# Optimization experiments

Hardware: AMD Instinct MI355X
Metric: run time of the kernel (lower is better)

Reference implementation:

```python
import jax, jax.numpy as jnp
import numpy as np

H, W = 32, 64          # img_size
NB = 4                 # fno_blocks
SCALE = 0.02


def setup_inputs() -> dict:
    key = jax.random.key(0)
    ks = jax.random.split(key, 8)
    B, N, C = 16, H * W, 768
    BS = C // NB
    x = jax.random.normal(ks[0], (B, N, C), dtype=jnp.float32)
    w1 = SCALE * jax.random.normal(ks[1], (2, NB, BS, BS), dtype=jnp.float32)
    b1 = SCALE * jax.random.normal(ks[2], (2, NB, BS), dtype=jnp.float32)
    w2 = SCALE * jax.random.normal(ks[3], (2, NB, BS, BS), dtype=jnp.float32)
    b2 = SCALE * jax.random.normal(ks[4], (2, NB, BS), dtype=jnp.float32)
    # Conv1d(C, C, kernel_size=1) == per-token linear layer over channels
    bias_w = jax.random.normal(ks[5], (C, C), dtype=jnp.float32) / np.sqrt(C)
    bias_b = jax.random.normal(ks[6], (C,), dtype=jnp.float32) * 0.01
    return {"x": x, "w1": w1, "b1": b1, "w2": w2, "b2": b2,
            "bias_w": bias_w, "bias_b": bias_b}


def _mul(a, w):
    # block-diagonal matmul: a [..., NB, BS], w [NB, BS, BS]
    return jnp.einsum('...bd,bdk->...bk', a, w)


def reference(x, w1, b1, w2, b2, bias_w, bias_b):
    B, N, C = x.shape
    BS = C // NB
    # Conv1d kernel-size-1 bias path
    bias = x @ bias_w.T + bias_b
    # spatial FFT
    xf = jnp.fft.rfftn(x.reshape(B, H, W, C), axes=(1, 2), norm='ortho')
    xf = xf.reshape(B, H, W // 2 + 1, NB, BS)
    xr, xi = xf.real, xf.imag
    # layer 1 (complex block-diag matmul + bias, ReLU on real/imag separately)
    r1 = jax.nn.relu(_mul(xr, w1[0]) - _mul(xi, w1[1]) + b1[0])
    i1 = jax.nn.relu(_mul(xr, w1[1]) + _mul(xi, w1[0]) + b1[1])
    # layer 2 -- NOTE: imag part uses the *updated* real part, matching the
    # original torch code's in-place reassignment order.
    r2 = _mul(r1, w2[0]) - _mul(i1, w2[1]) + b2[0]
    i2 = _mul(r2, w2[1]) + _mul(i1, w2[0]) + b2[1]
    xc = jax.lax.complex(r2, i2).reshape(B, H, W // 2 + 1, C)
    out = jnp.fft.irfftn(xc, s=(H, W), axes=(1, 2), norm='ortho')
    return out.reshape(B, N, C) + bias
```

## Files before the change

kernel.cpp:

```cpp
#include <hip/hip_runtime.h>
#include <hip/hip_bf16.h>
#include <stdint.h>

#define BB 16
#define HH 32
#define WW 64
#define CC 768
#define W2C 33
#define ROWW (2*CC)

typedef __bf16 bf16x8 __attribute__((ext_vector_type(8)));
typedef float f32x4 __attribute__((ext_vector_type(4)));

__device__ __forceinline__ unsigned short f2bf(float f) {
  __hip_bfloat16 h = __float2bfloat16(f);
  return __builtin_bit_cast(unsigned short, h);
}
__device__ __forceinline__ float bf2f(unsigned short u) {
  union { unsigned int i; float f; } x;
  x.i = ((unsigned int)u) << 16;
  return x.f;
}

__device__ __forceinline__ void g2l16(const void* g, void* l) {
  __builtin_amdgcn_global_load_lds((const __attribute__((address_space(1))) unsigned int*)g,
                                   (__attribute__((address_space(3))) unsigned int*)l,
                                   16, 0, 0);
}

__device__ __host__ constexpr int brevc(int x, int bits) {
  int r = 0;
  for (int i = 0; i < bits; ++i) r |= ((x >> i) & 1) << (bits - 1 - i);
  return r;
}

constexpr double TPI = 6.283185307179586476925286766559;
constexpr double tsin_(double x) {
  double t = x, s = x, x2 = x * x;
  for (int i = 1; i < 14; ++i) { t *= -x2 / (double)((2 * i) * (2 * i + 1)); s += t; }
  return s;
}
constexpr double tcos_(double x) {
  double t = 1.0, s = 1.0, x2 = x * x;
  for (int i = 1; i < 14; ++i) { t *= -x2 / (double)((2 * i - 1) * (2 * i)); s += t; }
  return s;
}
struct Tw64 { float c[64]; float s[64]; };
constexpr Tw64 mk_tw() {
  Tw64 r{};
  for (int k = 0; k < 64; ++k) {
    int q = k >> 4, m = k & 15;
    double a = (TPI / 64.0) * m;
    double cq = tcos_(a), sq = tsin_(a);
    double c, s;
    if (q == 0)      { c =  cq; s =  sq; }
    else if (q == 1) { c = -sq; s =  cq; }
    else if (q == 2) { c = -cq; s = -sq; }
    else             { c =  sq; s = -cq; }
    r.c[k] = (float)c;
    r.s[k] = (float)(-s);
  }
  return r;
}
constexpr Tw64 TW = mk_tw();

template<int N, bool INV>
__device__ __forceinline__ void fft_reg(float2 (&v)[N]) {
  constexpr int LOG2N = (N == 64) ? 6 : 5;
#pragma unroll
  for (int s = 0; s < LOG2N; ++s) {
    const int len = N >> s;
    const int half = len >> 1;
    const int tstep = 64 / len;
#pragma unroll
    for (int i = 0; i < N; i += len) {
#pragma unroll
      for (int j = 0; j < half; ++j) {
        float2 u = v[i + j];
        float2 t = v[i + j + half];
        float sr = u.x + t.x, si = u.y + t.y;
        float dr = u.x - t.x, di = u.y - t.y;
        float wr = TW.c[j * tstep];
        float wi = INV ? -TW.s[j * tstep] : TW.s[j * tstep];
        v[i + j] = make_float2(sr, si);
        v[i + j + half] = make_float2(dr * wr - di * wi, dr * wi + di * wr);
      }
    }
  }
}

__global__ __launch_bounds__(128) void fft_fwd_w(const float* __restrict__ x,
                                                 ushort2* __restrict__ yw,
                                                 unsigned short* __restrict__ xb) {
  __shared__ __align__(16) float xs[32][128];
  const int t = threadIdx.x;
  const int bh = blockIdx.x;
  const int c0 = blockIdx.y * 128;
  const float* xrow = x + (size_t)bh * (WW * CC) + c0;
  unsigned short* xbrow = xb + (size_t)bh * (WW * CC) + c0;
  const int rg = t >> 5;
  const int lc = (t & 31) * 4;
  float2 v[32];
#pragma unroll
  for (int half = 0; half < 2; ++half) {
    if (half) __syncthreads();
    float4 f[8];
#pragma unroll
    for (int it = 0; it < 8; ++it)
      f[it] = *(const float4*)(xrow + (size_t)(half * 32 + it * 4 + rg) * CC + lc);
#pragma unroll
    for (int it = 0; it < 8; ++it) {
      *(float4*)&xs[it * 4 + rg][lc] = f[it];
      *(ushort4*)(xbrow + (size_t)(half * 32 + it * 4 + rg) * CC + lc) =
          make_ushort4(f2bf(f[it].x), f2bf(f[it].y), f2bf(f[it].z), f2bf(f[it].w));
    }
    __syncthreads();
#pragma unroll
    for (int n = 0; n < 16; ++n)
      v[half * 16 + n] = make_float2(xs[2 * n][t], xs[2 * n + 1][t]);
  }
  fft_reg<32, false>(v);
  ushort2* yp = yw + (size_t)bh * (W2C * CC) + c0 + t;
  {
    float2 Z0 = v[0];
    yp[0] = make_ushort2(f2bf(Z0.x + Z0.y), f2bf(0.f));
    yp[(size_t)32 * CC] = make_ushort2(f2bf(Z0.x - Z0.y), f2bf(0.f));
  }
#pragma unroll
  for (int k = 1; k < 32; ++k) {
    float2 Zk = v[brevc(k, 5)];
    float2 Zm = v[brevc(32 - k, 5)];
    float Er = 0.5f * (Zk.x + Zm.x), Ei = 0.5f * (Zk.y - Zm.y);
    float Odr = 0.5f * (Zk.y + Zm.y), Odi = -0.5f * (Zk.x - Zm.x);
    float wx = TW.c[k], wy = TW.s[k];
    float Xr = Er + wx * Odr - wy * Odi;
    float Xi = Ei + wx * Odi + wy * Odr;
    yp[(size_t)k * CC] = make_ushort2(f2bf(Xr), f2bf(Xi));
  }
}

__global__ __launch_bounds__(256) void fft_fwd_h(const ushort2* __restrict__ yw,
                                                 unsigned short* __restrict__ xf) {
  const int bk = blockIdx.x;
  const int b = bk / W2C, kw = bk - b * W2C;
  const int c = blockIdx.y * 256 + threadIdx.x;
  const ushort2* yp = yw + ((size_t)b * HH * W2C + kw) * CC + c;
  float2 v[32];
#pragma unroll
  for (int h = 0; h < 32; ++h) {
    ushort2 u = yp[(size_t)h * (W2C * CC)];
    v[h] = make_float2(bf2f(u.x), bf2f(u.y));
  }
  fft_reg<32, false>(v);
  const int nb = c / 192, cc = c - nb * 192;
  unsigned short* xp = xf + (size_t)nb * 384 + cc;
  const float s = 0.022097086912079608f;
#pragma unroll
  for (int kh = 0; kh < 32; ++kh) {
    float2 z = v[brevc(kh, 5)];
    size_t m = ((size_t)b * HH + kh) * W2C + kw;
    xp[m * ROWW] = f2bf(z.x * s);
    xp[m * ROWW + 192] = f2bf(z.y * s);
  }
}

__global__ __launch_bounds__(256) void fft_inv_h(const unsigned short* __restrict__ r2,
                                                 ushort2* __restrict__ g) {
  const int bk = blockIdx.x;
  const int b = bk / W2C, kw = bk - b * W2C;
  const int c = blockIdx.y * 256 + threadIdx.x;
  const int nb = c / 192, cc = c - nb * 192;
  const unsigned short* rp = r2 + (size_t)nb * 384 + cc;
  float2 v[32];
#pragma unroll
  for (int kh = 0; kh < 32; ++kh) {
    size_t m = ((size_t)b * HH + kh) * W2C + kw;
    v[kh] = make_float2(bf2f(rp[m * ROWW]), bf2f(rp[m * ROWW + 192]));
  }
  fft_reg<32, true>(v);
  ushort2* gp = g + ((size_t)b * HH * W2C + kw) * CC + c;
#pragma unroll
  for (int h = 0; h < 32; ++h) {
    float2 z = v[brevc(h, 5)];
    gp[(size_t)h * (W2C * CC)] = make_ushort2(f2bf(z.x), f2bf(z.y));
  }
}

__global__ __launch_bounds__(128) void fft_inv_w(const ushort2* __restrict__ g,
                                                 const unsigned short* __restrict__ biasb,
                                                 float* __restrict__ out) {
  __shared__ __align__(16) float ys[32][128];
  const int t = threadIdx.x;
  const int bh = blockIdx.x;
  const int c0 = blockIdx.y * 128;
  const ushort2* gp = g + (size_t)bh * (W2C * CC) + c0 + t;
  float2 v[32];
  {
    float X0 = bf2f(gp[0].x);
    float X32 = bf2f(gp[(size_t)32 * CC].x);
    v[0] = make_float2(0.5f * (X0 + X32), 0.5f * (X0 - X32));
  }
#pragma unroll
  for (int k = 1; k < 32; ++k) {
    ushort2 uk = gp[(size_t)k * CC];
    ushort2 um = gp[(size_t)(32 - k) * CC];
    float2 Xk = make_float2(bf2f(uk.x), bf2f(uk.y));
    float2 Xm = make_float2(bf2f(um.x), bf2f(um.y));
    float Ar = 0.5f * (Xk.x + Xm.x), Ai = 0.5f * (Xk.y - Xm.y);
    float Dr = 0.5f * (Xk.x - Xm.x), Di = 0.5f * (Xk.y + Xm.y);
    float wx = TW.c[k], wy = TW.s[k];
    float Br = wx * Dr + wy * Di;
    float Bi = wx * Di - wy * Dr;
    v[k] = make_float2(Ar - Bi, Ai + Br);
  }
  fft_reg<32, true>(v);
  const float s2 = 0.04419417382415922f;
  float* orow = out + (size_t)bh * (WW * CC) + c0;
  const unsigned short* brow = biasb + (size_t)bh * (WW * CC) + c0;
  const int rg = t >> 5;
  const int lc = (t & 31) * 4;
#pragma unroll
  for (int half = 0; half < 2; ++half) {
    if (half) __syncthreads();
    ushort4 b4[8];
#pragma unroll
    for (int it = 0; it < 8; ++it)
      b4[it] = *(const ushort4*)(brow + (size_t)(half * 32 + it * 4 + rg) * CC + lc);
#pragma unroll
    for (int n = 0; n < 16; ++n) {
      float2 z = v[brevc(half * 16 + n, 5)];
      ys[2 * n][t] = z.x * s2;
      ys[2 * n + 1][t] = z.y * s2;
    }
    __syncthreads();
#pragma unroll
    for (int it = 0; it < 8; ++it) {
      const int w = half * 32 + it * 4 + rg;
      float4 f = *(const float4*)&ys[it * 4 + rg][lc];
      f.x += bf2f(b4[it].x); f.y += bf2f(b4[it].y);
      f.z += bf2f(b4[it].z); f.w += bf2f(b4[it].w);
      *(float4*)(orow + (size_t)w * CC + lc) = f;
    }
  }
}

template<bool RELU, bool OBF>
__global__ __launch_bounds__(256) void gemm_bt(
    const unsigned short* __restrict__ A, int lda, int aZ,
    const unsigned short* __restrict__ Bw, int K, int bZ,
    const float* __restrict__ bias, int biasZ,
    void* __restrict__ outp, int ldo, int oZ) {
  __shared__ __align__(16) unsigned short As[128 * 32];
  __shared__ __align__(16) unsigned short Bs[128 * 32];
  const int t = threadIdx.x;
  const int z = blockIdx.z;
  const size_t m0 = (size_t)blockIdx.x * 128;
  const int n0 = blockIdx.y * 128;
  const unsigned short* Ap = A + m0 * lda + (size_t)z * aZ;
  const unsigned short* Bp = Bw + (size_t)n0 * K + (size_t)z * bZ;
  const int lane = t & 63, wave = t >> 6;
  const int lr = lane & 15, quad = lane >> 4;
  const int wm = (wave >> 1) * 64, wn = (wave & 1) * 64;
  const int row = t >> 2;
  const int sl = t & 3;
  const int kb = (sl ^ ((row >> 1) & 3)) * 8;
  const int swzf = (lr >> 1) & 3;
  f32x4 acc[4][4] = {};
  for (int k0 = 0; k0 < K; k0 += 32) {
    const unsigned short* ga = Ap + (size_t)row * lda + (k0 + kb);
    g2l16(ga, &As[row * 32 + sl * 8]);
    g2l16(ga + (size_t)64 * lda, &As[(row + 64) * 32 + sl * 8]);
    const unsigned short* gb = Bp + (size_t)row * K + (k0 + kb);
    g2l16(gb, &Bs[row * 32 + sl * 8]);
    g2l16(gb + (size_t)64 * K, &Bs[(row + 64) * 32 + sl * 8]);
    __syncthreads();
    bf16x8 af[4], bfr[4];
#pragma unroll
    for (int mi = 0; mi < 4; ++mi)
      af[mi] = *(const bf16x8*)&As[(wm + mi * 16 + lr) * 32 + ((quad ^ swzf) * 8)];
#pragma unroll
    for (int ni = 0; ni < 4; ++ni)
      bfr[ni] = *(const bf16x8*)&Bs[(wn + ni * 16 + lr) * 32 + ((quad ^ swzf) * 8)];
#pragma unroll
    for (int mi = 0; mi < 4; ++mi)
#pragma unroll
      for (int ni = 0; ni < 4; ++ni)
        acc[mi][ni] = __builtin_amdgcn_mfma_f32_16x16x32_bf16(af[mi], bfr[ni], acc[mi][ni], 0, 0, 0);
    __syncthreads();
  }
#pragma unroll
  for (int mi = 0; mi < 4; ++mi) {
    const size_t mrow = m0 + wm + mi * 16 + quad * 4;
#pragma unroll
    for (int ni = 0; ni < 4; ++ni) {
      const int ncol = n0 + wn + ni * 16 + lr;
      const float bv = bias[z * biasZ + ncol];
#pragma unroll
      for (int r = 0; r < 4; ++r) {
        float vv = acc[mi][ni][r] + bv;
        if (RELU) vv = fmaxf(vv, 0.f);
        const size_t off = (mrow + r) * (size_t)ldo + (size_t)z * oZ + ncol;
        if (OBF) ((unsigned short*)outp)[off] = f2bf(vv);
        else ((float*)outp)[off] = vv;
      }
    }
  }
}

__global__ __launch_bounds__(256) void cvt_bf16(const float* __restrict__ in,
                                                unsigned short* __restrict__ outp) {
  const size_t i = ((size_t)blockIdx.x * 256 + threadIdx.x) * 4;
  float4 v = *(const float4*)(in + i);
  ushort4 o = make_ushort4(f2bf(v.x), f2bf(v.y), f2bf(v.z), f2bf(v.w));
  *(ushort4*)(outp + i) = o;
}

__global__ __launch_bounds__(256) void build_w1(const float* __restrict__ w1,
                                                const float* __restrict__ b1,
                                                unsigned short* __restrict__ w1t,
                                                float* __restrict__ bias1) {
  const int idx = blockIdx.x * 256 + threadIdx.x;
  const int nb = idx / (384 * 384);
  const int rem = idx - nb * (384 * 384);
  const int n = rem / 384, k = rem - (rem / 384) * 384;
  const bool khi = k >= 192, nhi = n >= 192;
  const int kk = khi ? k - 192 : k, nn = nhi ? n - 192 : n;
  float val;
  if (!khi && !nhi)      val =  w1[((0 * 4 + nb) * 192 + kk) * 192 + nn];
  else if (khi && !nhi)  val = -w1[((1 * 4 + nb) * 192 + kk) * 192 + nn];
  else if (!khi && nhi)  val =  w1[((1 * 4 + nb) * 192 + kk) * 192 + nn];
  else                   val =  w1[((0 * 4 + nb) * 192 + kk) * 192 + nn];
  w1t[((size_t)nb * 384 + n) * 384 + k] = f2bf(val);
  if (k == 0)
    bias1[nb * 384 + n] = nhi ? b1[(1 * 4 + nb) * 192 + nn] : b1[(0 * 4 + nb) * 192 + nn];
}

__global__ __launch_bounds__(256) void build_w2(const float* __restrict__ w2,
                                                const float* __restrict__ b2,
                                                unsigned short* __restrict__ w2t,
                                                float* __restrict__ bias2) {
  const int idx = blockIdx.x * 256 + threadIdx.x;
  const int nb = idx / (384 * 384);
  const int rem = idx - nb * (384 * 384);
  const int n = rem / 384, k = rem - (rem / 384) * 384;
  const bool khi = k >= 192, nhi = n >= 192;
  const int kk = khi ? k - 192 : k, nn = nhi ? n - 192 : n;
  float val;
  if (!khi && !nhi) {
    val = w2[((0 * 4 + nb) * 192 + kk) * 192 + nn];
  } else if (khi && !nhi) {
    val = -w2[((1 * 4 + nb) * 192 + kk) * 192 + nn];
  } else if (!khi && nhi) {
    float s = 0.f;
    for (int d = 0; d < 192; ++d)
      s += w2[((0 * 4 + nb) * 192 + kk) * 192 + d] * w2[((1 * 4 + nb) * 192 + d) * 192 + nn];
    val = s;
  } else {
    float s = 0.f;
    for (int d = 0; d < 192; ++d)
      s += w2[((1 * 4 + nb) * 192 + kk) * 192 + d] * w2[((1 * 4 + nb) * 192 + d) * 192 + nn];
    val = w2[((0 * 4 + nb) * 192 + kk) * 192 + nn] - s;
  }
  w2t[((size_t)nb * 384 + n) * 384 + k] = f2bf(val);
  if (k == 0) {
    float bv;
    if (!nhi) {
      bv = b2[(0 * 4 + nb) * 192 + nn];
    } else {
      float s = 0.f;
      for (int d = 0; d < 192; ++d)
        s += b2[(0 * 4 + nb) * 192 + d] * w2[((1 * 4 + nb) * 192 + d) * 192 + nn];
      bv = b2[(1 * 4 + nb) * 192 + nn] + s;
    }
    bias2[nb * 384 + n] = bv;
  }
}

extern "C" void kernel_launch(void* const* d_in, const int* in_sizes, int n_in,
                              void* d_out, int out_size, void* d_ws, size_t ws_size,
                              hipStream_t stream) {
  (void)in_sizes; (void)n_in; (void)out_size; (void)ws_size;
  const float* x  = (const float*)d_in[0];
  const float* w1 = (const float*)d_in[1];
  const float* b1 = (const float*)d_in[2];
  const float* w2 = (const float*)d_in[3];
  const float* b2 = (const float*)d_in[4];
  const float* bw = (const float*)d_in[5];
  const float* bb = (const float*)d_in[6];
  float* out = (float*)d_out;

  char* p = (char*)d_ws;
  unsigned short* buf1 = (unsigned short*)p; p += 51904512;
  unsigned short* buf2 = (unsigned short*)p; p += 51904512;
  unsigned short* buf3 = (unsigned short*)p; p += 51904512;
  unsigned short* bwb  = (unsigned short*)p; p += 1179648;
  unsigned short* w1t  = (unsigned short*)p; p += 1179648;
  unsigned short* w2t  = (unsigned short*)p; p += 1179648;
  float* bias1 = (float*)p; p += 6144;
  float* bias2 = (float*)p; p += 6144;

  cvt_bf16<<<589824 / 1024, 256, 0, stream>>>(bw, bwb);
  build_w1<<<589824 / 256, 256, 0, stream>>>(w1, b1, w1t, bias1);
  build_w2<<<589824 / 256, 256, 0, stream>>>(w2, b2, w2t, bias2);
  fft_fwd_w<<<dim3(BB * HH, 6), 128, 0, stream>>>(x, (ushort2*)buf1, buf2);
  gemm_bt<false, true><<<dim3(256, 6, 1), 256, 0, stream>>>(
      buf2, 768, 0, bwb, 768, 0, bb, 0, buf3, 768, 0);
  fft_fwd_h<<<dim3(BB * W2C, 3), 256, 0, stream>>>((const ushort2*)buf1, buf2);
  gemm_bt<true, true><<<dim3(132, 3, 4), 256, 0, stream>>>(
      buf2, ROWW, 384, w1t, 384, 384 * 384, bias1, 384, buf1, ROWW, 384);
  gemm_bt<false, true><<<dim3(132, 3, 4), 256, 0, stream>>>(
      buf1, ROWW, 384, w2t, 384, 384 * 384, bias2, 384, buf2, ROWW, 384);
  fft_inv_h<<<dim3(BB * W2C, 3), 256, 0, stream>>>(buf2, (ushort2*)buf1);
  fft_inv_w<<<dim3(BB * HH, 6), 128, 0, stream>>>((const ushort2*)buf1, buf3, out);
}
```

Baseline: 468.2 us.

## Double-buffer GEMM LDS tiles and interleave real/imag spectral layout

The GEMM main loop now uses two LDS stages, so the next K-tile is loaded while MFMAs run on the current one. This replaces the two barriers per iteration with one wait-and-barrier, and MFMA priority is raised around the compute block. Separately, the spectral buffer layout is changed so each channel's real and imaginary parts sit next to each other. The FFT H kernels can then read and write them as one ushort2 instead of two strided scalars, and the weight matrices and biases are permuted to match. Double buffering doubles the GEMM's LDS use, which may lower occupancy.

```diff
diff --git a/kernel.cpp b/kernel.cpp
--- a/kernel.cpp
+++ b/kernel.cpp
@@ -27,6 +27,9 @@
                                    (__attribute__((address_space(3))) unsigned int*)l,
                                    16, 0, 0);
 }
+
+#define WAITVM(n) asm volatile("s_waitcnt vmcnt(" #n ")" ::: "memory")
+#define MEMFENCE() asm volatile("" ::: "memory")
 
 __device__ __host__ constexpr int brevc(int x, int bits) {
   int r = 0;
@@ -153,14 +156,13 @@
   }
   fft_reg<32, false>(v);
   const int nb = c / 192, cc = c - nb * 192;
-  unsigned short* xp = xf + (size_t)nb * 384 + cc;
+  ushort2* xp = (ushort2*)(xf + (size_t)nb * 384 + 2 * cc);
   const float s = 0.022097086912079608f;
 #pragma unroll
   for (int kh = 0; kh < 32; ++kh) {
     float2 z = v[brevc(kh, 5)];
     size_t m = ((size_t)b * HH + kh) * W2C + kw;
-    xp[m * ROWW] = f2bf(z.x * s);
-    xp[m * ROWW + 192] = f2bf(z.y * s);
+    xp[m * (ROWW / 2)] = make_ushort2(f2bf(z.x * s), f2bf(z.y * s));
   }
 }
 
@@ -170,12 +172,13 @@
   const int b = bk / W2C, kw = bk - b * W2C;
   const int c = blockIdx.y * 256 + threadIdx.x;
   const int nb = c / 192, cc = c - nb * 192;
-  const unsigned short* rp = r2 + (size_t)nb * 384 + cc;
+  const ushort2* rp = (const ushort2*)(r2 + (size_t)nb * 384 + 2 * cc);
   float2 v[32];
 #pragma unroll
   for (int kh = 0; kh < 32; ++kh) {
     size_t m = ((size_t)b * HH + kh) * W2C + kw;
-    v[kh] = make_float2(bf2f(rp[m * ROWW]), bf2f(rp[m * ROWW + 192]));
+    ushort2 u = rp[m * (ROWW / 2)];
+    v[kh] = make_float2(bf2f(u.x), bf2f(u.y));
   }
   fft_reg<32, true>(v);
   ushort2* gp = g + ((size_t)b * HH * W2C + kw) * CC + c;
@@ -250,8 +253,8 @@
     const unsigned short* __restrict__ Bw, int K, int bZ,
     const float* __restrict__ bias, int biasZ,
     void* __restrict__ outp, int ldo, int oZ) {
-  __shared__ __align__(16) unsigned short As[128 * 32];
-  __shared__ __align__(16) unsigned short Bs[128 * 32];
+  __shared__ __align__(16) unsigned short As[2][128 * 32];
+  __shared__ __align__(16) unsigned short Bs[2][128 * 32];
   const int t = threadIdx.x;
   const int z = blockIdx.z;
   const size_t m0 = (size_t)blockIdx.x * 128;
@@ -265,29 +268,46 @@
   const int sl = t & 3;
   const int kb = (sl ^ ((row >> 1) & 3)) * 8;
   const int swzf = (lr >> 1) & 3;
+  const int NT = K >> 5;
   f32x4 acc[4][4] = {};
-  for (int k0 = 0; k0 < K; k0 += 32) {
-    const unsigned short* ga = Ap + (size_t)row * lda + (k0 + kb);
-    g2l16(ga, &As[row * 32 + sl * 8]);
-    g2l16(ga + (size_t)64 * lda, &As[(row + 64) * 32 + sl * 8]);
-    const unsigned short* gb = Bp + (size_t)row * K + (k0 + kb);
-    g2l16(gb, &Bs[row * 32 + sl * 8]);
-    g2l16(gb + (size_t)64 * K, &Bs[(row + 64) * 32 + sl * 8]);
-    __syncthreads();
+
+#define STG(k0_, s_) do { \
+    const unsigned short* ga_ = Ap + (size_t)row * lda + ((k0_) + kb); \
+    g2l16(ga_, &As[s_][row * 32 + sl * 8]); \
+    g2l16(ga_ + (size_t)64 * lda, &As[s_][(row + 64) * 32 + sl * 8]); \
+    const unsigned short* gb_ = Bp + (size_t)row * K + ((k0_) + kb); \
+    g2l16(gb_, &Bs[s_][row * 32 + sl * 8]); \
+    g2l16(gb_ + (size_t)64 * K, &Bs[s_][(row + 64) * 32 + sl * 8]); \
+  } while (0)
+
+  STG(0, 0);
+  WAITVM(0);
+  MEMFENCE(); __builtin_amdgcn_s_barrier(); MEMFENCE();
+  int cur = 0;
+  for (int tt = 0; tt < NT; ++tt) {
+    if (tt + 1 < NT) STG((tt + 1) * 32, cur ^ 1);
     bf16x8 af[4], bfr[4];
 #pragma unroll
     for (int mi = 0; mi < 4; ++mi)
-      af[mi] = *(const bf16x8*)&As[(wm + mi * 16 + lr) * 32 + ((quad ^ swzf) * 8)];
+      af[mi] = *(const bf16x8*)&As[cur][(wm + mi * 16 + lr) * 32 + ((quad ^ swzf) * 8)];
 #pragma unroll
     for (int ni = 0; ni < 4; ++ni)
-      bfr[ni] = *(const bf16x8*)&Bs[(wn + ni * 16 + lr) * 32 + ((quad ^ swzf) * 8)];
+      bfr[ni] = *(const bf16x8*)&Bs[cur][(wn + ni * 16 + lr) * 32 + ((quad ^ swzf) * 8)];
+    __builtin_amdgcn_s_setprio(1);
 #pragma unroll
     for (int mi = 0; mi < 4; ++mi)
 #pragma unroll
       for (int ni = 0; ni < 4; ++ni)
         acc[mi][ni] = __builtin_amdgcn_mfma_f32_16x16x32_bf16(af[mi], bfr[ni], acc[mi][ni], 0, 0, 0);
-    __syncthreads();
-  }
+    __builtin_amdgcn_s_setprio(0);
+    if (tt + 1 < NT) {
+      WAITVM(0);
+      MEMFENCE(); __builtin_amdgcn_s_barrier(); MEMFENCE();
+      cur ^= 1;
+    }
+  }
+#undef STG
+
 #pragma unroll
   for (int mi = 0; mi < 4; ++mi) {
     const size_t mrow = m0 + wm + mi * 16 + quad * 4;
@@ -330,9 +350,11 @@
   else if (khi && !nhi)  val = -w1[((1 * 4 + nb) * 192 + kk) * 192 + nn];
   else if (!khi && nhi)  val =  w1[((1 * 4 + nb) * 192 + kk) * 192 + nn];
   else                   val =  w1[((0 * 4 + nb) * 192 + kk) * 192 + nn];
-  w1t[((size_t)nb * 384 + n) * 384 + k] = f2bf(val);
+  const int k2 = 2 * kk + (khi ? 1 : 0);
+  const int n2 = 2 * nn + (nhi ? 1 : 0);
+  w1t[((size_t)nb * 384 + n2) * 384 + k2] = f2bf(val);
   if (k == 0)
-    bias1[nb * 384 + n] = nhi ? b1[(1 * 4 + nb) * 192 + nn] : b1[(0 * 4 + nb) * 192 + nn];
+    bias1[nb * 384 + n2] = nhi ? b1[(1 * 4 + nb) * 192 + nn] : b1[(0 * 4 + nb) * 192 + nn];
 }
 
 __global__ __launch_bounds__(256) void build_w2(const float* __restrict__ w2,
@@ -361,7 +383,9 @@
       s += w2[((1 * 4 + nb) * 192 + kk) * 192 + d] * w2[((1 * 4 + nb) * 192 + d) * 192 + nn];
     val = w2[((0 * 4 + nb) * 192 + kk) * 192 + nn] - s;
   }
-  w2t[((size_t)nb * 384 + n) * 384 + k] = f2bf(val);
+  const int k2 = 2 * kk + (khi ? 1 : 0);
+  const int n2 = 2 * nn + (nhi ? 1 : 0);
+  w2t[((size_t)nb * 384 + n2) * 384 + k2] = f2bf(val);
   if (k == 0) {
     float bv;
     if (!nhi) {
@@ -372,7 +396,7 @@
         s += b2[(0 * 4 + nb) * 192 + d] * w2[((1 * 4 + nb) * 192 + d) * 192 + nn];
       bv = b2[(1 * 4 + nb) * 192 + nn] + s;
     }
-    bias2[nb * 384 + n] = bv;
+    bias2[nb * 384 + n2] = bv;
   }
 }
 
```

Measured after the change: 469.7 us. About the same (+0.3%).
